# Kernel optimization log

Hardware: AMD Instinct MI355X
Metric: run time of the kernel (lower is better)

## Reference

```python
import jax, jax.numpy as jnp
import numpy as np

D = 1024   # 'heads' arg = d_model
H = 4      # no_of_heads
DH = D // H
B, T = 4, 2048


def _ln(x, g, b, eps=1e-5):
    m = x.mean(-1, keepdims=True)
    v = ((x - m) ** 2).mean(-1, keepdims=True)
    return (x - m) / jnp.sqrt(v + eps) * g + b


def _heads_proj(x, W):
    # x: [B,T,D]; W: [H,dh,dh] per-head nn.Linear weights (out = x @ W^T)
    b, t, c = x.shape
    h, dh, _ = W.shape
    xh = x.reshape(b, t, h, dh)  # channel slices i*dh:(i+1)*dh == reshape
    return jnp.einsum('bthd,hed->bthe', xh, W)


def _self_attn(x, wq, wk, wv, masked):
    q = _heads_proj(x, wq)
    k = _heads_proj(x, wk)
    v = _heads_proj(x, wv)
    dh = wq.shape[-1]
    s = jnp.einsum('bthe,bshe->bhts', q, k) * dh ** -0.5  # [B,H,T,T]
    if masked:
        t = x.shape[1]
        causal = jnp.tril(jnp.ones((t, t), dtype=bool))
        s = jnp.where(causal, s, -jnp.inf)
    a = jax.nn.softmax(s, axis=-1)
    o = jnp.einsum('bhts,bshd->bthd', a, v)
    return o.reshape(x.shape)


def _cross_attn(ctx, x, wq, wk, wv):
    # NOTE: the original CrossAttention applies NO softmax — faithful copy.
    q = _heads_proj(x, wq)
    k = _heads_proj(ctx, wk)
    v = _heads_proj(ctx, wv)
    dh = wq.shape[-1]
    s = jnp.einsum('bthe,bshe->bhts', q, k) * dh ** -0.5
    o = jnp.einsum('bhts,bshd->bthd', s, v)
    return o.reshape(x.shape)


def _ffn(x, w1, b1, w2, b2):
    return jax.nn.relu(x @ w1.T + b1) @ w2.T + b2


def setup_inputs() -> dict:
    key = jax.random.key(0)
    ks = jax.random.split(key, 16)
    sc = 0.02
    d = {
        'context': jax.random.normal(ks[0], (B, T, D), jnp.float32),
        'X': jax.random.normal(ks[1], (B, T, D), jnp.float32),
        'dec_wq': jax.random.normal(ks[2], (H, DH, DH), jnp.float32) * sc,
        'dec_wk': jax.random.normal(ks[3], (H, DH, DH), jnp.float32) * sc,
        'dec_wv': jax.random.normal(ks[4], (H, DH, DH), jnp.float32) * sc,
        'x_wq': jax.random.normal(ks[5], (H, DH, DH), jnp.float32) * sc,
        'x_wk': jax.random.normal(ks[6], (H, DH, DH), jnp.float32) * sc,
        'x_wv': jax.random.normal(ks[7], (H, DH, DH), jnp.float32) * sc,
        'enc_wq': jax.random.normal(ks[8], (H, DH, DH), jnp.float32) * sc,
        'enc_wk': jax.random.normal(ks[9], (H, DH, DH), jnp.float32) * sc,
        'enc_wv': jax.random.normal(ks[10], (H, DH, DH), jnp.float32) * sc,
        'dec_w1': jax.random.normal(ks[11], (4 * D, D), jnp.float32) * sc,
        'dec_b1': jnp.zeros((4 * D,), jnp.float32),
        'dec_w2': jax.random.normal(ks[12], (D, 4 * D), jnp.float32) * sc,
        'dec_b2': jnp.zeros((D,), jnp.float32),
        'enc_w1': jax.random.normal(ks[13], (4 * D, D), jnp.float32) * sc,
        'enc_b1': jnp.zeros((4 * D,), jnp.float32),
        'enc_w2': jax.random.normal(ks[14], (D, 4 * D), jnp.float32) * sc,
        'enc_b2': jnp.zeros((D,), jnp.float32),
        'dec_ln1_g': jnp.ones((D,), jnp.float32), 'dec_ln1_b': jnp.zeros((D,), jnp.float32),
        'dec_ln2_g': jnp.ones((D,), jnp.float32), 'dec_ln2_b': jnp.zeros((D,), jnp.float32),
        'dec_ln3_g': jnp.ones((D,), jnp.float32), 'dec_ln3_b': jnp.zeros((D,), jnp.float32),
        'enc_ln1_g': jnp.ones((D,), jnp.float32), 'enc_ln1_b': jnp.zeros((D,), jnp.float32),
        'enc_ln2_g': jnp.ones((D,), jnp.float32), 'enc_ln2_b': jnp.zeros((D,), jnp.float32),
    }
    return d


def reference(context, X, dec_wq, dec_wk, dec_wv, x_wq, x_wk, x_wv,
              enc_wq, enc_wk, enc_wv, dec_w1, dec_b1, dec_w2, dec_b2,
              enc_w1, enc_b1, enc_w2, enc_b2,
              dec_ln1_g, dec_ln1_b, dec_ln2_g, dec_ln2_b, dec_ln3_g, dec_ln3_b,
              enc_ln1_g, enc_ln1_b, enc_ln2_g, enc_ln2_b):
    # Dropout (p=0.1) treated as identity (eval mode).
    x1 = _ln(X + _self_attn(X, dec_wq, dec_wk, dec_wv, True), dec_ln1_g, dec_ln1_b)
    # EncoderBlock on context (non-masked self-attn + FFN)
    c = _ln(context + _self_attn(context, enc_wq, enc_wk, enc_wv, False), enc_ln1_g, enc_ln1_b)
    c = _ln(c + _ffn(c, enc_w1, enc_b1, enc_w2, enc_b2), enc_ln2_g, enc_ln2_b)
    x2 = _ln(x1 + _cross_attn(c, x1, x_wq, x_wk, x_wv), dec_ln2_g, dec_ln2_b)
    out = _ln(x2 + _ffn(x2, dec_w1, dec_b1, dec_w2, dec_b2), dec_ln3_g, dec_ln3_b)
    return (c, out)
```

## Files before the change

### kernel.cpp

```cpp
#include <hip/hip_runtime.h>
#include <hip/hip_bf16.h>

typedef unsigned short u16;
typedef __bf16 bf16x8 __attribute__((ext_vector_type(8)));
typedef unsigned short u16x8 __attribute__((ext_vector_type(8)));
typedef unsigned short u16x4 __attribute__((ext_vector_type(4)));
typedef float f32x4 __attribute__((ext_vector_type(4)));

#define DI static __device__ __forceinline__

DI u16 f2bf(float f) {
    unsigned u = __builtin_bit_cast(unsigned, f);
    u += 0x7FFFu + ((u >> 16) & 1u);
    return (u16)(u >> 16);
}
DI float bf2f(u16 u) {
    unsigned x = ((unsigned)u) << 16;
    return __builtin_bit_cast(float, x);
}
DI u16x8 ld8_f32(const float* __restrict__ p) {
    const float4 a = *(const float4*)p;
    const float4 b = *(const float4*)(p + 4);
    u16x8 r = { f2bf(a.x), f2bf(a.y), f2bf(a.z), f2bf(a.w),
                f2bf(b.x), f2bf(b.y), f2bf(b.z), f2bf(b.w) };
    return r;
}
DI f32x4 mfma16(u16x8 a, u16x8 b, f32x4 c) {
    return __builtin_amdgcn_mfma_f32_16x16x32_bf16(
        __builtin_bit_cast(bf16x8, a), __builtin_bit_cast(bf16x8, b), c, 0, 0, 0);
}

__global__ void __launch_bounds__(256) k_cast(const float* __restrict__ in,
                                              u16* __restrict__ out, long n4) {
    long i = (long)blockIdx.x * 256 + threadIdx.x;
    if (i >= n4) return;
    const float4 v = *(const float4*)(in + i * 4);
    u16x4 o = { f2bf(v.x), f2bf(v.y), f2bf(v.z), f2bf(v.w) };
    *(u16x4*)(out + i * 4) = o;
}

template <int AF32, int BF32>
__global__ void __launch_bounds__(256, 2) k_gemm_bt(
    const void* __restrict__ Ap, long lda,
    const void* __restrict__ Bp, long ldb,
    float* __restrict__ Cf, u16* __restrict__ Cb, long ldc,
    const float* __restrict__ bias, int relu, int accum, float alpha, int K,
    int Hdiv, long sAb, long sAh, long sBb, long sBh, long sCb, long sCh)
{
    __shared__ __align__(16) u16 As[2][128 * 72];
    __shared__ __align__(16) u16 Bs[2][128 * 72];
    const int tid  = threadIdx.x;
    const int lane = tid & 63, wave = tid >> 6;
    const int r16  = lane & 15, quad = lane >> 4;
    const int wr   = (wave >> 1) * 64, wc = (wave & 1) * 64;
    const int zb = blockIdx.z / Hdiv, zh = blockIdx.z % Hdiv;
    const long aoff = (long)zb * sAb + (long)zh * sAh + (long)blockIdx.x * 128 * lda;
    const long boff = (long)zb * sBb + (long)zh * sBh + (long)blockIdx.y * 128 * ldb;
    const u16*   A16 = (const u16*)Ap + aoff;
    const float* A32 = (const float*)Ap + aoff;
    const u16*   B16 = (const u16*)Bp + boff;
    const float* B32 = (const float*)Bp + boff;
    const long coff = (long)zb * sCb + (long)zh * sCh +
                      (long)blockIdx.x * 128 * ldc + (long)blockIdx.y * 128;

    f32x4 acc[4][4];
#pragma unroll
    for (int i = 0; i < 4; i++)
#pragma unroll
        for (int j = 0; j < 4; j++) acc[i][j] = f32x4{0.f, 0.f, 0.f, 0.f};

    const int st_row = tid >> 3;
    const int st_col = (tid & 7) * 8;

    u16x8 ar0, ar1, ar2, ar3, br0, br1, br2, br3;

#define LDAB(KS)                                                              \
    do {                                                                      \
        const long kk0_ = (long)(KS) * 64 + st_col;                           \
        if constexpr (AF32) {                                                 \
            ar0 = ld8_f32(A32 + (long)(st_row)      * lda + kk0_);            \
            ar1 = ld8_f32(A32 + (long)(st_row + 32) * lda + kk0_);            \
            ar2 = ld8_f32(A32 + (long)(st_row + 64) * lda + kk0_);            \
            ar3 = ld8_f32(A32 + (long)(st_row + 96) * lda + kk0_);            \
        } else {                                                              \
            ar0 = *(const u16x8*)(A16 + (long)(st_row)      * lda + kk0_);    \
            ar1 = *(const u16x8*)(A16 + (long)(st_row + 32) * lda + kk0_);    \
            ar2 = *(const u16x8*)(A16 + (long)(st_row + 64) * lda + kk0_);    \
            ar3 = *(const u16x8*)(A16 + (long)(st_row + 96) * lda + kk0_);    \
        }                                                                     \
        if constexpr (BF32) {                                                 \
            br0 = ld8_f32(B32 + (long)(st_row)      * ldb + kk0_);            \
            br1 = ld8_f32(B32 + (long)(st_row + 32) * ldb + kk0_);            \
            br2 = ld8_f32(B32 + (long)(st_row + 64) * ldb + kk0_);            \
            br3 = ld8_f32(B32 + (long)(st_row + 96) * ldb + kk0_);            \
        } else {                                                              \
            br0 = *(const u16x8*)(B16 + (long)(st_row)      * ldb + kk0_);    \
            br1 = *(const u16x8*)(B16 + (long)(st_row + 32) * ldb + kk0_);    \
            br2 = *(const u16x8*)(B16 + (long)(st_row + 64) * ldb + kk0_);    \
            br3 = *(const u16x8*)(B16 + (long)(st_row + 96) * ldb + kk0_);    \
        }                                                                     \
    } while (0)

#define STAB(P)                                                               \
    do {                                                                      \
        u16* ap_ = As[P] + st_row * 72 + st_col;                              \
        *(u16x8*)(ap_)            = ar0;                                      \
        *(u16x8*)(ap_ + 32 * 72)  = ar1;                                      \
        *(u16x8*)(ap_ + 64 * 72)  = ar2;                                      \
        *(u16x8*)(ap_ + 96 * 72)  = ar3;                                      \
        u16* bp_ = Bs[P] + st_row * 72 + st_col;                              \
        *(u16x8*)(bp_)            = br0;                                      \
        *(u16x8*)(bp_ + 32 * 72)  = br1;                                      \
        *(u16x8*)(bp_ + 64 * 72)  = br2;                                      \
        *(u16x8*)(bp_ + 96 * 72)  = br3;                                      \
    } while (0)

    LDAB(0);
    STAB(0);
    __syncthreads();

    const int nks = K >> 6;
    int p = 0;
    for (int ks = 0; ks < nks; ks++) {
        const bool more = (ks + 1 < nks);
        if (more) LDAB(ks + 1);
        const u16* as_ = As[p];
        const u16* bs_ = Bs[p];
#pragma unroll
        for (int kk = 0; kk < 64; kk += 32) {
            u16x8 af[4], bfr[4];
#pragma unroll
            for (int i = 0; i < 4; i++)
                af[i] = *(const u16x8*)(as_ + (wr + i * 16 + r16) * 72 + kk + 8 * quad);
#pragma unroll
            for (int j = 0; j < 4; j++)
                bfr[j] = *(const u16x8*)(bs_ + (wc + j * 16 + r16) * 72 + kk + 8 * quad);
#pragma unroll
            for (int i = 0; i < 4; i++)
#pragma unroll
                for (int j = 0; j < 4; j++)
                    acc[i][j] = mfma16(af[i], bfr[j], acc[i][j]);
        }
        if (more) {
            STAB(p ^ 1);
            __syncthreads();
        }
        p ^= 1;
    }
#undef LDAB
#undef STAB

#pragma unroll
    for (int i = 0; i < 4; i++) {
#pragma unroll
        for (int j = 0; j < 4; j++) {
            const int gcol = wc + j * 16 + r16;
            const float bv = bias ? bias[blockIdx.y * 128 + gcol] : 0.f;
#pragma unroll
            for (int r = 0; r < 4; r++) {
                const long o = coff + (long)(wr + i * 16 + quad * 4 + r) * ldc + gcol;
                float v = acc[i][j][r] * alpha + bv;
                if (accum) v += Cf[o];
                if (relu) v = fmaxf(v, 0.f);
                if (Cf) Cf[o] = v;
                if (Cb) Cb[o] = f2bf(v);
            }
        }
    }
}

template <int NSEG>
__global__ void __launch_bounds__(256) k_proj(
    const float* __restrict__ A,
    const float* __restrict__ W0, const float* __restrict__ W1,
    const float* __restrict__ W2,
    u16* __restrict__ C0, u16* __restrict__ C1, u16* __restrict__ C2)
{
    __shared__ __align__(16) u16 As[128 * 72];
    __shared__ __align__(16) u16 Bs[128 * 72];
    const int tid  = threadIdx.x;
    const int lane = tid & 63, wave = tid >> 6;
    const int r16  = lane & 15, quad = lane >> 4;
    const int wr   = (wave >> 1) * 64, wc = (wave & 1) * 64;
    const int seg = blockIdx.y >> 1, yy = blockIdx.y & 1, h = blockIdx.z;
    const float* W = (NSEG >= 3 && seg == 2) ? W2 : (seg == 1 ? W1 : W0);
    u16*         C = (NSEG >= 3 && seg == 2) ? C2 : (seg == 1 ? C1 : C0);
    const float* Ab = A + (long)blockIdx.x * 128 * 1024 + h * 256;
    const float* Bb = W + (long)h * 65536 + yy * 128 * 256;
    u16* Cp = C + (long)blockIdx.x * 128 * 1024 + h * 256 + yy * 128;

    f32x4 acc[4][4];
#pragma unroll
    for (int i = 0; i < 4; i++)
#pragma unroll
        for (int j = 0; j < 4; j++) acc[i][j] = f32x4{0.f, 0.f, 0.f, 0.f};

    const int st_row = tid >> 3, st_col = (tid & 7) * 8;

    for (int k0 = 0; k0 < 256; k0 += 64) {
#pragma unroll
        for (int r = 0; r < 4; r++) {
            const int row = st_row + 32 * r;
            *(u16x8*)(As + row * 72 + st_col) = ld8_f32(Ab + (long)row * 1024 + k0 + st_col);
            *(u16x8*)(Bs + row * 72 + st_col) = ld8_f32(Bb + (long)row * 256 + k0 + st_col);
        }
        __syncthreads();
#pragma unroll
        for (int kk = 0; kk < 64; kk += 32) {
            u16x8 af[4], bfr[4];
#pragma unroll
            for (int i = 0; i < 4; i++)
                af[i] = *(const u16x8*)(As + (wr + i * 16 + r16) * 72 + kk + 8 * quad);
#pragma unroll
            for (int j = 0; j < 4; j++)
                bfr[j] = *(const u16x8*)(Bs + (wc + j * 16 + r16) * 72 + kk + 8 * quad);
#pragma unroll
            for (int i = 0; i < 4; i++)
#pragma unroll
                for (int j = 0; j < 4; j++)
                    acc[i][j] = mfma16(af[i], bfr[j], acc[i][j]);
        }
        __syncthreads();
    }

#pragma unroll
    for (int i = 0; i < 4; i++)
#pragma unroll
        for (int j = 0; j < 4; j++)
#pragma unroll
            for (int r = 0; r < 4; r++)
                Cp[(long)(wr + i * 16 + quad * 4 + r) * 1024 + wc + j * 16 + r16] =
                    f2bf(acc[i][j][r]);
}

template <int MASKED>
__global__ void __launch_bounds__(512, 2) k_attn(
    const u16* __restrict__ Q, const u16* __restrict__ Kg, const u16* __restrict__ Vt,
    u16* __restrict__ O, int T, float scale)
{
    const int D = 1024;
    __shared__ __align__(16) u16 Ks[2][64 * 264];
    __shared__ __align__(16) u16 VsT[2][256 * 72];
    __shared__ __align__(16) u16 Ps[8][16 * 72];
    const int tid = threadIdx.x, lane = tid & 63, wave = tid >> 6;
    const int r16 = lane & 15, quad = lane >> 4;

    const int fid = blockIdx.x;
    const int swz = ((fid & 7) << 5) | (fid >> 3);
    const int bx = swz & 15, hh = (swz >> 4) & 3, bb = swz >> 6;

    const long base   = ((long)bb * T) * D + hh * 256;
    const long vtbase = ((long)(bb * 4 + hh) * 256) * 2048;
    const int qr0 = bx * 128 + wave * 16;

    u16x8 qf[8];
#pragma unroll
    for (int ks = 0; ks < 8; ks++)
        qf[ks] = *(const u16x8*)(Q + base + (long)(qr0 + r16) * D + ks * 32 + 8 * quad);

    f32x4 oacc[16];
#pragma unroll
    for (int nt = 0; nt < 16; nt++) oacc[nt] = f32x4{0.f, 0.f, 0.f, 0.f};
    f32x4 lacc = f32x4{0.f, 0.f, 0.f, 0.f};
    const u16x8 ones8 = {0x3F80, 0x3F80, 0x3F80, 0x3F80,
                         0x3F80, 0x3F80, 0x3F80, 0x3F80};

    const int krow = tid >> 5, kcol = (tid & 31) * 8;
    const int vrow = tid >> 3, vcol = (tid & 7) * 8;
    const int nkb = MASKED ? (2 * bx + 2) : (T / 64);

    const u16* kg = Kg + base;
    const u16* vg = Vt + vtbase + (long)vrow * 2048 + vcol;

    uint4 kr0, kr1, kr2, kr3, vr0, vr1, vr2, vr3;

#define LD_KV(KB)                                                          \
    do {                                                                   \
        const u16* kp_ = kg + ((long)(KB) * 64 + krow) * D + kcol;         \
        kr0 = *(const uint4*)(kp_);                                        \
        kr1 = *(const uint4*)(kp_ + 16 * D);                               \
        kr2 = *(const uint4*)(kp_ + 32 * D);                               \
        kr3 = *(const uint4*)(kp_ + 48 * D);                               \
        const u16* vp_ = vg + (KB) * 64;                                   \
        vr0 = *(const uint4*)(vp_);                                        \
        vr1 = *(const uint4*)(vp_ + 64 * 2048);                            \
        vr2 = *(const uint4*)(vp_ + 128 * 2048);                           \
        vr3 = *(const uint4*)(vp_ + 192 * 2048);                           \
    } while (0)

#define ST_KV(P)                                                           \
    do {                                                                   \
        u16* kq_ = Ks[P] + krow * 264 + kcol;                              \
        *(uint4*)(kq_)            = kr0;                                   \
        *(uint4*)(kq_ + 16 * 264) = kr1;                                   \
        *(uint4*)(kq_ + 32 * 264) = kr2;                                   \
        *(uint4*)(kq_ + 48 * 264) = kr3;                                   \
        u16* vq_ = VsT[P] + vrow * 72 + vcol;                              \
        *(uint4*)(vq_)            = vr0;                                   \
        *(uint4*)(vq_ + 64 * 72)  = vr1;                                   \
        *(uint4*)(vq_ + 128 * 72) = vr2;                                   \
        *(uint4*)(vq_ + 192 * 72) = vr3;                                   \
    } while (0)

    LD_KV(0);
    ST_KV(0);
    __syncthreads();

    u16* const pw = &Ps[wave][0];
    int p = 0;

    for (int kb = 0; kb < nkb; kb++) {
        const bool more = (kb + 1 < nkb);
        if (more) LD_KV(kb + 1);

        const u16* ks_ = Ks[p];
        const u16* vs_ = VsT[p];

        f32x4 s0 = f32x4{0.f,0.f,0.f,0.f}, s1 = f32x4{0.f,0.f,0.f,0.f};
        f32x4 s2 = f32x4{0.f,0.f,0.f,0.f}, s3 = f32x4{0.f,0.f,0.f,0.f};
        __builtin_amdgcn_s_setprio(1);
#pragma unroll
        for (int ks = 0; ks < 8; ks++) {
            const u16x8 a = qf[ks];
            const u16* kp = ks_ + r16 * 264 + ks * 32 + 8 * quad;
            s0 = mfma16(a, *(const u16x8*)(kp),            s0);
            s1 = mfma16(a, *(const u16x8*)(kp + 16 * 264), s1);
            s2 = mfma16(a, *(const u16x8*)(kp + 32 * 264), s2);
            s3 = mfma16(a, *(const u16x8*)(kp + 48 * 264), s3);
        }
        __builtin_amdgcn_s_setprio(0);

        const bool domask = MASKED && (kb * 64 + 63 > qr0);

#pragma unroll
        for (int r = 0; r < 4; r++) {
            float a0 = s0[r] * scale, a1 = s1[r] * scale;
            float a2 = s2[r] * scale, a3 = s3[r] * scale;
            if (domask) {
                const int qi = qr0 + quad * 4 + r;
                const int kb0 = kb * 64;
                if (kb0 + r16 > qi)      a0 = -1e30f;
                if (kb0 + 16 + r16 > qi) a1 = -1e30f;
                if (kb0 + 32 + r16 > qi) a2 = -1e30f;
                if (kb0 + 48 + r16 > qi) a3 = -1e30f;
            }
            const float p0 = __expf(fminf(a0, 30.f));
            const float p1 = __expf(fminf(a1, 30.f));
            const float p2 = __expf(fminf(a2, 30.f));
            const float p3 = __expf(fminf(a3, 30.f));
            u16* pr = pw + (quad * 4 + r) * 72 + r16;
            pr[0]  = f2bf(p0);
            pr[16] = f2bf(p1);
            pr[32] = f2bf(p2);
            pr[48] = f2bf(p3);
        }

        const u16* pp = pw + r16 * 72 + 8 * quad;
        const u16x8 pfA = *(const u16x8*)(pp);
        const u16x8 pfB = *(const u16x8*)(pp + 32);
        __builtin_amdgcn_s_setprio(1);
        lacc = mfma16(pfA, ones8, lacc);
        lacc = mfma16(pfB, ones8, lacc);
#pragma unroll
        for (int nt = 0; nt < 16; nt++) {
            const u16* vp = vs_ + (nt * 16 + r16) * 72 + 8 * quad;
            oacc[nt] = mfma16(pfA, *(const u16x8*)(vp),      oacc[nt]);
            oacc[nt] = mfma16(pfB, *(const u16x8*)(vp + 32), oacc[nt]);
        }
        __builtin_amdgcn_s_setprio(0);

        if (more) {
            ST_KV(p ^ 1);
            __syncthreads();
        }
        p ^= 1;
    }
#undef LD_KV
#undef ST_KV

#pragma unroll
    for (int r = 0; r < 4; r++) lacc[r] = 1.f / lacc[r];
#pragma unroll
    for (int nt = 0; nt < 16; nt++)
#pragma unroll
        for (int r = 0; r < 4; r++)
            O[base + (long)(qr0 + quad * 4 + r) * D + nt * 16 + r16] =
                f2bf(oacc[nt][r] * lacc[r]);
}

template <int XF32, int RF32>
__global__ void __launch_bounds__(256) k_addln(
    const void* __restrict__ Xp, const void* __restrict__ Rp,
    const float* __restrict__ G, const float* __restrict__ Bv,
    float* __restrict__ Yf, u16* __restrict__ Yb)
{
    const int tid = threadIdx.x;
    const long off = (long)blockIdx.x * 1024 + tid * 4;
    float v[4];
    if constexpr (XF32) {
        const float4 a = *(const float4*)((const float*)Xp + off);
        v[0] = a.x; v[1] = a.y; v[2] = a.z; v[3] = a.w;
    } else {
        const u16x4 a = *(const u16x4*)((const u16*)Xp + off);
        v[0] = bf2f(a[0]); v[1] = bf2f(a[1]); v[2] = bf2f(a[2]); v[3] = bf2f(a[3]);
    }
    if constexpr (RF32) {
        const float4 b = *(const float4*)((const float*)Rp + off);
        v[0] += b.x; v[1] += b.y; v[2] += b.z; v[3] += b.w;
    } else {
        const u16x4 b = *(const u16x4*)((const u16*)Rp + off);
        v[0] += bf2f(b[0]); v[1] += bf2f(b[1]); v[2] += bf2f(b[2]); v[3] += bf2f(b[3]);
    }
    float s1 = v[0] + v[1] + v[2] + v[3];
    float s2 = v[0]*v[0] + v[1]*v[1] + v[2]*v[2] + v[3]*v[3];
#pragma unroll
    for (int m = 1; m < 64; m <<= 1) { s1 += __shfl_xor(s1, m); s2 += __shfl_xor(s2, m); }
    __shared__ float red[8];
    if ((tid & 63) == 0) { red[(tid >> 6) * 2] = s1; red[(tid >> 6) * 2 + 1] = s2; }
    __syncthreads();
    s1 = red[0] + red[2] + red[4] + red[6];
    s2 = red[1] + red[3] + red[5] + red[7];
    const float mean = s1 * (1.f / 1024.f);
    const float rstd = rsqrtf(s2 * (1.f / 1024.f) - mean * mean + 1e-5f);
    const float4 g  = *(const float4*)(G + tid * 4);
    const float4 be = *(const float4*)(Bv + tid * 4);
    const float o0 = (v[0] - mean) * rstd * g.x + be.x;
    const float o1 = (v[1] - mean) * rstd * g.y + be.y;
    const float o2 = (v[2] - mean) * rstd * g.z + be.z;
    const float o3 = (v[3] - mean) * rstd * g.w + be.w;
    if (Yf) { float4 of = {o0, o1, o2, o3}; *(float4*)(Yf + off) = of; }
    if (Yb) { u16x4 ob = {f2bf(o0), f2bf(o1), f2bf(o2), f2bf(o3)}; *(u16x4*)(Yb + off) = ob; }
}

__global__ void __launch_bounds__(256) k_transpose(const u16* __restrict__ Xin,
                                                   u16* __restrict__ Y)
{
    __shared__ u16 tile[32][33];
    const int tx = threadIdx.x & 31, ty = threadIdx.x >> 5;
    const int t0 = blockIdx.x * 32, e0 = blockIdx.y * 32, bh = blockIdx.z;
    const int b = bh >> 2, h = bh & 3;
#pragma unroll
    for (int i = 0; i < 4; i++)
        tile[ty + 8 * i][tx] =
            Xin[((long)(b * 2048 + t0 + ty + 8 * i)) * 1024 + h * 256 + e0 + tx];
    __syncthreads();
#pragma unroll
    for (int i = 0; i < 4; i++)
        Y[((long)bh * 256 + e0 + ty + 8 * i) * 2048 + t0 + tx] = tile[tx][ty + 8 * i];
}

#define GEMM(AF, BF, Aptr, lda, Bptr, ldb, pCf, pCb, ldc, bias, relu, accum, alpha, \
             M, N, K, Z, Hdiv, sAb, sAh, sBb, sBh, sCb, sCh)                        \
    k_gemm_bt<AF, BF><<<dim3((M) / 128, (N) / 128, (Z)), dim3(256), 0, stream>>>(   \
        (const void*)(Aptr), (lda), (const void*)(Bptr), (ldb), (pCf), (pCb),       \
        (ldc), (bias), (relu), (accum), (alpha), (K), (Hdiv),                       \
        (long)(sAb), (long)(sAh), (long)(sBb), (long)(sBh), (long)(sCb), (long)(sCh))

extern "C" void kernel_launch(void* const* d_in, const int* in_sizes, int n_in,
                              void* d_out, int out_size, void* d_ws, size_t ws_size,
                              hipStream_t stream)
{
    const int Bn = 4, T = 2048, D = 1024, H = 4, DH = 256;
    const long BTD = (long)Bn * T * D;
    const long MB = 1024 * 1024;

    const float* ctx = (const float*)d_in[0];
    const float* X   = (const float*)d_in[1];
    const float* Wh[9]; for (int i = 0; i < 9; i++) Wh[i] = (const float*)d_in[2 + i];
    const float* dec_w1 = (const float*)d_in[11]; const float* dec_b1 = (const float*)d_in[12];
    const float* dec_w2 = (const float*)d_in[13]; const float* dec_b2 = (const float*)d_in[14];
    const float* enc_w1 = (const float*)d_in[15]; const float* enc_b1 = (const float*)d_in[16];
    const float* enc_w2 = (const float*)d_in[17]; const float* enc_b2 = (const float*)d_in[18];
    const float* ln[10]; for (int i = 0; i < 10; i++) ln[i] = (const float*)d_in[19 + i];
    (void)in_sizes; (void)n_in; (void)out_size; (void)ws_size;

    float* outC = (float*)d_out;
    float* outY = (float*)d_out + BTD;

    char* w = (char*)d_ws;
    u16*   qb   = (u16*)(w);
    u16*   kb   = (u16*)(w + 16 * MB);
    u16*   vb   = (u16*)(w + 32 * MB);
    u16*   tmpB = (u16*)(w + 48 * MB);
    float* fout = (float*)(w);
    u16*   w1b  = (u16*)(w + 16 * MB);
    u16*   w2b  = (u16*)(w + 24 * MB);
    u16*   hb   = (u16*)(w + 32 * MB);
    u16*   Kt2  = (u16*)(w + 32 * MB);
    u16*   crossO= (u16*)(w + 32 * MB);
    u16*   Vt2  = (u16*)(w + 48 * MB);
    u16*   Nm   = (u16*)(w + 64 * MB);
    u16*   x1b  = (u16*)(w + 66 * MB);
    u16*   t2b  = (u16*)(w + 82 * MB);

    k_proj<3><<<dim3(64, 6, 4), dim3(256), 0, stream>>>(
        X, Wh[0], Wh[1], Wh[2], qb, kb, vb);
    k_transpose<<<dim3(T / 32, DH / 32, Bn * H), dim3(256), 0, stream>>>(vb, tmpB);
    k_attn<1><<<dim3(256), dim3(512), 0, stream>>>(qb, kb, tmpB, vb, T, 0.0625f);
    k_addln<1, 0><<<dim3(Bn * T), dim3(256), 0, stream>>>(X, vb, ln[0], ln[1], nullptr, x1b);

    k_proj<3><<<dim3(64, 6, 4), dim3(256), 0, stream>>>(
        ctx, Wh[6], Wh[7], Wh[8], qb, kb, vb);
    k_transpose<<<dim3(T / 32, DH / 32, Bn * H), dim3(256), 0, stream>>>(vb, tmpB);
    k_attn<0><<<dim3(256), dim3(512), 0, stream>>>(qb, kb, tmpB, vb, T, 0.0625f);
    k_addln<1, 0><<<dim3(Bn * T), dim3(256), 0, stream>>>(ctx, vb, ln[6], ln[7], nullptr, t2b);

    k_cast<<<dim3(4096), dim3(256), 0, stream>>>(enc_w1, w1b, 1048576);
    k_cast<<<dim3(4096), dim3(256), 0, stream>>>(enc_w2, w2b, 1048576);
    for (int c = 0; c < 2; c++) {
        const long moff = (long)c * 4096 * 1024;
        GEMM(0, 0, t2b + moff, D, w1b, D, nullptr, hb, 4096, enc_b1, 1, 0, 1.f,
             4096, 4096, 1024, 1, 1, 0, 0, 0, 0, 0, 0);
        GEMM(0, 0, hb, 4096, w2b, 4096, fout, nullptr, 1024, enc_b2, 0, 0, 1.f,
             4096, 1024, 4096, 1, 1, 0, 0, 0, 0, 0, 0);
        k_addln<0, 1><<<dim3(4096), dim3(256), 0, stream>>>(
            t2b + moff, fout, ln[8], ln[9], outC + moff, nullptr);
    }

    GEMM(0, 1, x1b, D, Wh[3], DH, nullptr, qb, D, nullptr, 0, 0, 1.f,
         Bn * T, DH, DH, H, H, 0, DH, 0, DH * DH, 0, DH);
    k_proj<2><<<dim3(64, 4, 4), dim3(256), 0, stream>>>(
        outC, Wh[4], Wh[5], nullptr, kb, t2b, nullptr);
    k_transpose<<<dim3(T / 32, DH / 32, Bn * H), dim3(256), 0, stream>>>(kb, Kt2);
    k_transpose<<<dim3(T / 32, DH / 32, Bn * H), dim3(256), 0, stream>>>(t2b, Vt2);
    GEMM(0, 0, Vt2, T, Kt2, T, nullptr, Nm, DH, nullptr, 0, 0, 1.f,
         DH, DH, T, Bn * H, Bn * H, 0, (long)DH * T, 0, (long)DH * T, 0, DH * DH);
    GEMM(0, 0, qb, D, Nm, DH, nullptr, crossO, D, nullptr, 0, 0, 0.0625f,
         T, DH, DH, Bn * H, H, (long)T * D, DH, (long)H * DH * DH, DH * DH,
         (long)T * D, DH);
    k_addln<0, 0><<<dim3(Bn * T), dim3(256), 0, stream>>>(x1b, crossO, ln[2], ln[3], nullptr, t2b);

    k_cast<<<dim3(4096), dim3(256), 0, stream>>>(dec_w1, w1b, 1048576);
    k_cast<<<dim3(4096), dim3(256), 0, stream>>>(dec_w2, w2b, 1048576);
    for (int c = 0; c < 2; c++) {
        const long moff = (long)c * 4096 * 1024;
        GEMM(0, 0, t2b + moff, D, w1b, D, nullptr, hb, 4096, dec_b1, 1, 0, 1.f,
             4096, 4096, 1024, 1, 1, 0, 0, 0, 0, 0, 0);
        GEMM(0, 0, hb, 4096, w2b, 4096, fout, nullptr, 1024, dec_b2, 0, 0, 1.f,
             4096, 1024, 4096, 1, 1, 0, 0, 0, 0, 0, 0);
        k_addln<0, 1><<<dim3(4096), dim3(256), 0, stream>>>(
            t2b + moff, fout, ln[4], ln[5], outY + moff, nullptr);
    }
}
```

Baseline: 958.2 us.

## Add direct global-to-LDS FFN GEMM kernel with swizzled double buffering

Adds a dedicated bf16 GEMM kernel for the encoder and decoder FFN matmuls. It loads tiles straight from global memory into LDS with global_load_lds, uses an XOR-swizzled unpadded layout, keeps two K-tiles in flight with explicit vmcnt waits, and raises wave priority around the MFMA block. The intent is to cut register staging and load latency in the dominant GEMMs. The generic GEMM is also changed to use a single LDS buffer with an extra barrier, which lowers its LDS use but may reduce overlap for the remaining projections.

Result: no change. 967.9 us (+1.0%).

```diff
diff --git a/kernel.cpp b/kernel.cpp
--- a/kernel.cpp
+++ b/kernel.cpp
@@ -28,6 +28,12 @@
 DI f32x4 mfma16(u16x8 a, u16x8 b, f32x4 c) {
     return __builtin_amdgcn_mfma_f32_16x16x32_bf16(
         __builtin_bit_cast(bf16x8, a), __builtin_bit_cast(bf16x8, b), c, 0, 0, 0);
+}
+
+typedef __attribute__((address_space(1))) const unsigned int as1_u32;
+typedef __attribute__((address_space(3))) unsigned int as3_u32;
+DI void gload_lds16(const u16* g, u16* l) {
+    __builtin_amdgcn_global_load_lds((as1_u32*)g, (as3_u32*)l, 16, 0, 0);
 }
 
 __global__ void __launch_bounds__(256) k_cast(const float* __restrict__ in,
@@ -37,6 +43,104 @@
     const float4 v = *(const float4*)(in + i * 4);
     u16x4 o = { f2bf(v.x), f2bf(v.y), f2bf(v.z), f2bf(v.w) };
     *(u16x4*)(out + i * 4) = o;
+}
+
+__global__ void __launch_bounds__(256, 2) k_ffn(
+    const u16* __restrict__ A, long lda,
+    const u16* __restrict__ B, long ldb,
+    float* __restrict__ Cf, u16* __restrict__ Cb, long ldc,
+    const float* __restrict__ bias, int relu, int K)
+{
+    __shared__ __align__(16) u16 As[2][128 * 64];
+    __shared__ __align__(16) u16 Bs[2][128 * 64];
+    const int tid = threadIdx.x, lane = tid & 63, wave = tid >> 6;
+    const int r16 = lane & 15, quad = lane >> 4;
+    const int wr = (wave >> 1) * 64, wc = (wave & 1) * 64;
+    const u16* Ab = A + (long)blockIdx.x * 128 * lda;
+    const u16* Bb = B + (long)blockIdx.y * 128 * ldb;
+    const long coff = (long)blockIdx.x * 128 * ldc + blockIdx.y * 128;
+
+    f32x4 acc[4][4];
+#pragma unroll
+    for (int i = 0; i < 4; i++)
+#pragma unroll
+        for (int j = 0; j < 4; j++) acc[i][j] = f32x4{0.f, 0.f, 0.f, 0.f};
+
+    const int srow = tid >> 3;
+    const int dcol = (tid & 7) * 8;
+    const int scol = dcol ^ ((srow & 7) << 3);
+    const int xorv = (r16 & 7) << 3;
+
+#define STAGE(P, KT)                                                       \
+    do {                                                                   \
+        const long kc_ = (long)(KT) * 64 + scol;                           \
+        _Pragma("unroll")                                                  \
+        for (int i_ = 0; i_ < 4; i_++)                                     \
+            gload_lds16(Ab + (long)(i_ * 32 + srow) * lda + kc_,           \
+                        As[P] + (i_ * 32 + srow) * 64 + dcol);             \
+        _Pragma("unroll")                                                  \
+        for (int i_ = 0; i_ < 4; i_++)                                     \
+            gload_lds16(Bb + (long)(i_ * 32 + srow) * ldb + kc_,           \
+                        Bs[P] + (i_ * 32 + srow) * 64 + dcol);             \
+    } while (0)
+
+    const int nkt = K >> 6;
+    STAGE(0, 0);
+    STAGE(1, 1);
+    asm volatile("s_waitcnt vmcnt(8)" ::: "memory");
+    __builtin_amdgcn_sched_barrier(0);
+    __builtin_amdgcn_s_barrier();
+
+    for (int kt = 0; kt < nkt; kt++) {
+        const u16* as_ = As[kt & 1];
+        const u16* bs_ = Bs[kt & 1];
+        __builtin_amdgcn_s_setprio(1);
+#pragma unroll
+        for (int kk = 0; kk < 64; kk += 32) {
+            u16x8 af[4], bfr[4];
+#pragma unroll
+            for (int i = 0; i < 4; i++)
+                af[i] = *(const u16x8*)(as_ + (wr + i * 16 + r16) * 64 +
+                                        ((kk + 8 * quad) ^ xorv));
+#pragma unroll
+            for (int j = 0; j < 4; j++)
+                bfr[j] = *(const u16x8*)(bs_ + (wc + j * 16 + r16) * 64 +
+                                         ((kk + 8 * quad) ^ xorv));
+#pragma unroll
+            for (int i = 0; i < 4; i++)
+#pragma unroll
+                for (int j = 0; j < 4; j++)
+                    acc[i][j] = mfma16(af[i], bfr[j], acc[i][j]);
+        }
+        __builtin_amdgcn_s_setprio(0);
+        __builtin_amdgcn_s_barrier();
+        if (kt + 2 < nkt) {
+            STAGE(kt & 1, kt + 2);
+            asm volatile("s_waitcnt vmcnt(8)" ::: "memory");
+        } else {
+            asm volatile("s_waitcnt vmcnt(0)" ::: "memory");
+        }
+        __builtin_amdgcn_sched_barrier(0);
+        if (kt + 1 < nkt) __builtin_amdgcn_s_barrier();
+    }
+#undef STAGE
+
+#pragma unroll
+    for (int i = 0; i < 4; i++) {
+#pragma unroll
+        for (int j = 0; j < 4; j++) {
+            const int gcol = wc + j * 16 + r16;
+            const float bv = bias ? bias[blockIdx.y * 128 + gcol] : 0.f;
+#pragma unroll
+            for (int r = 0; r < 4; r++) {
+                const long o = coff + (long)(wr + i * 16 + quad * 4 + r) * ldc + gcol;
+                float v = acc[i][j][r] + bv;
+                if (relu) v = fmaxf(v, 0.f);
+                if (Cf) Cf[o] = v;
+                if (Cb) Cb[o] = f2bf(v);
+            }
+        }
+    }
 }
 
 template <int AF32, int BF32>
@@ -47,8 +151,8 @@
     const float* __restrict__ bias, int relu, int accum, float alpha, int K,
     int Hdiv, long sAb, long sAh, long sBb, long sBh, long sCb, long sCh)
 {
-    __shared__ __align__(16) u16 As[2][128 * 72];
-    __shared__ __align__(16) u16 Bs[2][128 * 72];
+    __shared__ __align__(16) u16 As[128 * 72];
+    __shared__ __align__(16) u16 Bs[128 * 72];
     const int tid  = threadIdx.x;
     const int lane = tid & 63, wave = tid >> 6;
     const int r16  = lane & 15, quad = lane >> 4;
@@ -101,14 +205,14 @@
         }                                                                     \
     } while (0)
 
-#define STAB(P)                                                               \
+#define STAB()                                                                \
     do {                                                                      \
-        u16* ap_ = As[P] + st_row * 72 + st_col;                              \
+        u16* ap_ = As + st_row * 72 + st_col;                                 \
         *(u16x8*)(ap_)            = ar0;                                      \
         *(u16x8*)(ap_ + 32 * 72)  = ar1;                                      \
         *(u16x8*)(ap_ + 64 * 72)  = ar2;                                      \
         *(u16x8*)(ap_ + 96 * 72)  = ar3;                                      \
-        u16* bp_ = Bs[P] + st_row * 72 + st_col;                              \
+        u16* bp_ = Bs + st_row * 72 + st_col;                                 \
         *(u16x8*)(bp_)            = br0;                                      \
         *(u16x8*)(bp_ + 32 * 72)  = br1;                                      \
         *(u16x8*)(bp_ + 64 * 72)  = br2;                                      \
@@ -116,36 +220,33 @@
     } while (0)
 
     LDAB(0);
-    STAB(0);
+    STAB();
     __syncthreads();
 
     const int nks = K >> 6;
-    int p = 0;
     for (int ks = 0; ks < nks; ks++) {
         const bool more = (ks + 1 < nks);
         if (more) LDAB(ks + 1);
-        const u16* as_ = As[p];
-        const u16* bs_ = Bs[p];
 #pragma unroll
         for (int kk = 0; kk < 64; kk += 32) {
             u16x8 af[4], bfr[4];
 #pragma unroll
             for (int i = 0; i < 4; i++)
-                af[i] = *(const u16x8*)(as_ + (wr + i * 16 + r16) * 72 + kk + 8 * quad);
+                af[i] = *(const u16x8*)(As + (wr + i * 16 + r16) * 72 + kk + 8 * quad);
 #pragma unroll
             for (int j = 0; j < 4; j++)
-                bfr[j] = *(const u16x8*)(bs_ + (wc + j * 16 + r16) * 72 + kk + 8 * quad);
+                bfr[j] = *(const u16x8*)(Bs + (wc + j * 16 + r16) * 72 + kk + 8 * quad);
 #pragma unroll
             for (int i = 0; i < 4; i++)
 #pragma unroll
                 for (int j = 0; j < 4; j++)
                     acc[i][j] = mfma16(af[i], bfr[j], acc[i][j]);
         }
+        __syncthreads();
         if (more) {
-            STAB(p ^ 1);
+            STAB();
             __syncthreads();
         }
-        p ^= 1;
     }
 #undef LDAB
 #undef STAB
@@ -509,10 +610,10 @@
     k_cast<<<dim3(4096), dim3(256), 0, stream>>>(enc_w2, w2b, 1048576);
     for (int c = 0; c < 2; c++) {
         const long moff = (long)c * 4096 * 1024;
-        GEMM(0, 0, t2b + moff, D, w1b, D, nullptr, hb, 4096, enc_b1, 1, 0, 1.f,
-             4096, 4096, 1024, 1, 1, 0, 0, 0, 0, 0, 0);
-        GEMM(0, 0, hb, 4096, w2b, 4096, fout, nullptr, 1024, enc_b2, 0, 0, 1.f,
-             4096, 1024, 4096, 1, 1, 0, 0, 0, 0, 0, 0);
+        k_ffn<<<dim3(32, 32), dim3(256), 0, stream>>>(
+            t2b + moff, D, w1b, D, nullptr, hb, 4096, enc_b1, 1, 1024);
+        k_ffn<<<dim3(32, 8), dim3(256), 0, stream>>>(
+            hb, 4096, w2b, 4096, fout, nullptr, 1024, enc_b2, 0, 4096);
         k_addln<0, 1><<<dim3(4096), dim3(256), 0, stream>>>(
             t2b + moff, fout, ln[8], ln[9], outC + moff, nullptr);
     }
@@ -534,10 +635,10 @@
     k_cast<<<dim3(4096), dim3(256), 0, stream>>>(dec_w2, w2b, 1048576);
     for (int c = 0; c < 2; c++) {
         const long moff = (long)c * 4096 * 1024;
-        GEMM(0, 0, t2b + moff, D, w1b, D, nullptr, hb, 4096, dec_b1, 1, 0, 1.f,
-             4096, 4096, 1024, 1, 1, 0, 0, 0, 0, 0, 0);
-        GEMM(0, 0, hb, 4096, w2b, 4096, fout, nullptr, 1024, dec_b2, 0, 0, 1.f,
-             4096, 1024, 4096, 1, 1, 0, 0, 0, 0, 0, 0);
+        k_ffn<<<dim3(32, 32), dim3(256), 0, stream>>>(
+            t2b + moff, D, w1b, D, nullptr, hb, 4096, dec_b1, 1, 1024);
+        k_ffn<<<dim3(32, 8), dim3(256), 0, stream>>>(
+            hb, 4096, w2b, 4096, fout, nullptr, 1024, dec_b2, 0, 4096);
         k_addln<0, 1><<<dim3(4096), dim3(256), 0, stream>>>(
             t2b + moff, fout, ln[4], ln[5], outY + moff, nullptr);
     }
```

## Balance causal attention by pairing query strips; single-buffer GEMM shared memory

Applied to the files above, without the earlier changes.

The causal attention kernel now gives each block two 64-row query strips, one from the start and one from the end of the sequence, so every block does about the same number of key blocks instead of a triangular spread. Waves skip tiles past their own strip, and masking is applied only on the diagonal tile. Separately, the GEMM drops its double-buffered shared memory for a single buffer with an extra barrier, which halves LDS use and may raise occupancy but serializes the LDS store against compute.

Measured after the change: 925.2 us. 1.04x faster.

```diff
diff --git a/kernel.cpp b/kernel.cpp
--- a/kernel.cpp
+++ b/kernel.cpp
@@ -47,8 +47,8 @@
     const float* __restrict__ bias, int relu, int accum, float alpha, int K,
     int Hdiv, long sAb, long sAh, long sBb, long sBh, long sCb, long sCh)
 {
-    __shared__ __align__(16) u16 As[2][128 * 72];
-    __shared__ __align__(16) u16 Bs[2][128 * 72];
+    __shared__ __align__(16) u16 As[128 * 72];
+    __shared__ __align__(16) u16 Bs[128 * 72];
     const int tid  = threadIdx.x;
     const int lane = tid & 63, wave = tid >> 6;
     const int r16  = lane & 15, quad = lane >> 4;
@@ -101,14 +101,14 @@
         }                                                                     \
     } while (0)
 
-#define STAB(P)                                                               \
+#define STAB()                                                                \
     do {                                                                      \
-        u16* ap_ = As[P] + st_row * 72 + st_col;                              \
+        u16* ap_ = As + st_row * 72 + st_col;                                 \
         *(u16x8*)(ap_)            = ar0;                                      \
         *(u16x8*)(ap_ + 32 * 72)  = ar1;                                      \
         *(u16x8*)(ap_ + 64 * 72)  = ar2;                                      \
         *(u16x8*)(ap_ + 96 * 72)  = ar3;                                      \
-        u16* bp_ = Bs[P] + st_row * 72 + st_col;                              \
+        u16* bp_ = Bs + st_row * 72 + st_col;                                 \
         *(u16x8*)(bp_)            = br0;                                      \
         *(u16x8*)(bp_ + 32 * 72)  = br1;                                      \
         *(u16x8*)(bp_ + 64 * 72)  = br2;                                      \
@@ -116,36 +116,33 @@
     } while (0)
 
     LDAB(0);
-    STAB(0);
+    STAB();
     __syncthreads();
 
     const int nks = K >> 6;
-    int p = 0;
     for (int ks = 0; ks < nks; ks++) {
         const bool more = (ks + 1 < nks);
         if (more) LDAB(ks + 1);
-        const u16* as_ = As[p];
-        const u16* bs_ = Bs[p];
 #pragma unroll
         for (int kk = 0; kk < 64; kk += 32) {
             u16x8 af[4], bfr[4];
 #pragma unroll
             for (int i = 0; i < 4; i++)
-                af[i] = *(const u16x8*)(as_ + (wr + i * 16 + r16) * 72 + kk + 8 * quad);
+                af[i] = *(const u16x8*)(As + (wr + i * 16 + r16) * 72 + kk + 8 * quad);
 #pragma unroll
             for (int j = 0; j < 4; j++)
-                bfr[j] = *(const u16x8*)(bs_ + (wc + j * 16 + r16) * 72 + kk + 8 * quad);
+                bfr[j] = *(const u16x8*)(Bs + (wc + j * 16 + r16) * 72 + kk + 8 * quad);
 #pragma unroll
             for (int i = 0; i < 4; i++)
 #pragma unroll
                 for (int j = 0; j < 4; j++)
                     acc[i][j] = mfma16(af[i], bfr[j], acc[i][j]);
         }
+        __syncthreads();
         if (more) {
-            STAB(p ^ 1);
+            STAB();
             __syncthreads();
         }
-        p ^= 1;
     }
 #undef LDAB
 #undef STAB
@@ -247,11 +244,22 @@
 
     const int fid = blockIdx.x;
     const int swz = ((fid & 7) << 5) | (fid >> 3);
-    const int bx = swz & 15, hh = (swz >> 4) & 3, bb = swz >> 6;
+    const int grp = swz & 15, hh = (swz >> 4) & 3, bb = swz >> 6;
+
+    int qr0, nkb, myMax;
+    if (MASKED) {
+        const int strip = (wave < 4) ? grp : (31 - grp);
+        qr0   = strip * 64 + (wave & 3) * 16;
+        myMax = strip;
+        nkb   = 32 - grp;
+    } else {
+        qr0   = grp * 128 + wave * 16;
+        myMax = 1 << 30;
+        nkb   = T / 64;
+    }
 
     const long base   = ((long)bb * T) * D + hh * 256;
     const long vtbase = ((long)(bb * 4 + hh) * 256) * 2048;
-    const int qr0 = bx * 128 + wave * 16;
 
     u16x8 qf[8];
 #pragma unroll
@@ -267,7 +275,6 @@
 
     const int krow = tid >> 5, kcol = (tid & 31) * 8;
     const int vrow = tid >> 3, vcol = (tid & 7) * 8;
-    const int nkb = MASKED ? (2 * bx + 2) : (T / 64);
 
     const u16* kg = Kg + base;
     const u16* vg = Vt + vtbase + (long)vrow * 2048 + vcol;
@@ -313,61 +320,63 @@
         const bool more = (kb + 1 < nkb);
         if (more) LD_KV(kb + 1);
 
-        const u16* ks_ = Ks[p];
-        const u16* vs_ = VsT[p];
-
-        f32x4 s0 = f32x4{0.f,0.f,0.f,0.f}, s1 = f32x4{0.f,0.f,0.f,0.f};
-        f32x4 s2 = f32x4{0.f,0.f,0.f,0.f}, s3 = f32x4{0.f,0.f,0.f,0.f};
-        __builtin_amdgcn_s_setprio(1);
-#pragma unroll
-        for (int ks = 0; ks < 8; ks++) {
-            const u16x8 a = qf[ks];
-            const u16* kp = ks_ + r16 * 264 + ks * 32 + 8 * quad;
-            s0 = mfma16(a, *(const u16x8*)(kp),            s0);
-            s1 = mfma16(a, *(const u16x8*)(kp + 16 * 264), s1);
-            s2 = mfma16(a, *(const u16x8*)(kp + 32 * 264), s2);
-            s3 = mfma16(a, *(const u16x8*)(kp + 48 * 264), s3);
-        }
-        __builtin_amdgcn_s_setprio(0);
-
-        const bool domask = MASKED && (kb * 64 + 63 > qr0);
-
-#pragma unroll
-        for (int r = 0; r < 4; r++) {
-            float a0 = s0[r] * scale, a1 = s1[r] * scale;
-            float a2 = s2[r] * scale, a3 = s3[r] * scale;
-            if (domask) {
-                const int qi = qr0 + quad * 4 + r;
-                const int kb0 = kb * 64;
-                if (kb0 + r16 > qi)      a0 = -1e30f;
-                if (kb0 + 16 + r16 > qi) a1 = -1e30f;
-                if (kb0 + 32 + r16 > qi) a2 = -1e30f;
-                if (kb0 + 48 + r16 > qi) a3 = -1e30f;
+        if (!MASKED || kb <= myMax) {
+            const u16* ks_ = Ks[p];
+            const u16* vs_ = VsT[p];
+
+            f32x4 s0 = f32x4{0.f,0.f,0.f,0.f}, s1 = f32x4{0.f,0.f,0.f,0.f};
+            f32x4 s2 = f32x4{0.f,0.f,0.f,0.f}, s3 = f32x4{0.f,0.f,0.f,0.f};
+            __builtin_amdgcn_s_setprio(1);
+#pragma unroll
+            for (int ks = 0; ks < 8; ks++) {
+                const u16x8 a = qf[ks];
+                const u16* kp = ks_ + r16 * 264 + ks * 32 + 8 * quad;
+                s0 = mfma16(a, *(const u16x8*)(kp),            s0);
+                s1 = mfma16(a, *(const u16x8*)(kp + 16 * 264), s1);
+                s2 = mfma16(a, *(const u16x8*)(kp + 32 * 264), s2);
+                s3 = mfma16(a, *(const u16x8*)(kp + 48 * 264), s3);
             }
-            const float p0 = __expf(fminf(a0, 30.f));
-            const float p1 = __expf(fminf(a1, 30.f));
-            const float p2 = __expf(fminf(a2, 30.f));
-            const float p3 = __expf(fminf(a3, 30.f));
-            u16* pr = pw + (quad * 4 + r) * 72 + r16;
-            pr[0]  = f2bf(p0);
-            pr[16] = f2bf(p1);
-            pr[32] = f2bf(p2);
-            pr[48] = f2bf(p3);
-        }
-
-        const u16* pp = pw + r16 * 72 + 8 * quad;
-        const u16x8 pfA = *(const u16x8*)(pp);
-        const u16x8 pfB = *(const u16x8*)(pp + 32);
-        __builtin_amdgcn_s_setprio(1);
-        lacc = mfma16(pfA, ones8, lacc);
-        lacc = mfma16(pfB, ones8, lacc);
-#pragma unroll
-        for (int nt = 0; nt < 16; nt++) {
-            const u16* vp = vs_ + (nt * 16 + r16) * 72 + 8 * quad;
-            oacc[nt] = mfma16(pfA, *(const u16x8*)(vp),      oacc[nt]);
-            oacc[nt] = mfma16(pfB, *(const u16x8*)(vp + 32), oacc[nt]);
-        }
-        __builtin_amdgcn_s_setprio(0);
+            __builtin_amdgcn_s_setprio(0);
+
+            const bool domask = MASKED && (kb == myMax);
+
+#pragma unroll
+            for (int r = 0; r < 4; r++) {
+                float a0 = s0[r] * scale, a1 = s1[r] * scale;
+                float a2 = s2[r] * scale, a3 = s3[r] * scale;
+                if (domask) {
+                    const int qi = qr0 + quad * 4 + r;
+                    const int kb0 = kb * 64;
+                    if (kb0 + r16 > qi)      a0 = -1e30f;
+                    if (kb0 + 16 + r16 > qi) a1 = -1e30f;
+                    if (kb0 + 32 + r16 > qi) a2 = -1e30f;
+                    if (kb0 + 48 + r16 > qi) a3 = -1e30f;
+                }
+                const float p0 = __expf(fminf(a0, 30.f));
+                const float p1 = __expf(fminf(a1, 30.f));
+                const float p2 = __expf(fminf(a2, 30.f));
+                const float p3 = __expf(fminf(a3, 30.f));
+                u16* pr = pw + (quad * 4 + r) * 72 + r16;
+                pr[0]  = f2bf(p0);
+                pr[16] = f2bf(p1);
+                pr[32] = f2bf(p2);
+                pr[48] = f2bf(p3);
+            }
+
+            const u16* pp = pw + r16 * 72 + 8 * quad;
+            const u16x8 pfA = *(const u16x8*)(pp);
+            const u16x8 pfB = *(const u16x8*)(pp + 32);
+            __builtin_amdgcn_s_setprio(1);
+            lacc = mfma16(pfA, ones8, lacc);
+            lacc = mfma16(pfB, ones8, lacc);
+#pragma unroll
+            for (int nt = 0; nt < 16; nt++) {
+                const u16* vp = vs_ + (nt * 16 + r16) * 72 + 8 * quad;
+                oacc[nt] = mfma16(pfA, *(const u16x8*)(vp),      oacc[nt]);
+                oacc[nt] = mfma16(pfB, *(const u16x8*)(vp + 32), oacc[nt]);
+            }
+            __builtin_amdgcn_s_setprio(0);
+        }
 
         if (more) {
             ST_KV(p ^ 1);
```
